# Optimization experiments

Hardware: AMD Instinct MI355X
Metric: run time of the kernel (lower is better)

## Reference

```python
import jax, jax.numpy as jnp
import numpy as np

B = 16            # batch of graphs
N = 512           # n_node
D = 32            # embedding_dim
MAXN = 16         # max_neighbors
E = MAXN * (N - 1)   # 8176 edges per graph
SLEFT = N * D
FSS = 601         # full_support_size
NA = N - 1        # num_actions (so one-hot rows == B*n_node)
IN0 = D + 1       # sa feature dim
NTOT = B * N


def _gat(x, snd, rcv, W, a_src, a_dst, b):
    # single-head GATConv, add_self_loops=False
    h = x @ W                                            # [BN, C]
    e = (h * a_src).sum(-1)[snd] + (h * a_dst).sum(-1)[rcv]
    e = jnp.where(e > 0, e, 0.2 * e)                     # LeakyReLU(0.2)
    m = jax.ops.segment_max(e, rcv, num_segments=NTOT)   # segment softmax
    m = jnp.where(jnp.isfinite(m), m, 0.0)
    ee = jnp.exp(e - m[rcv])
    den = jax.ops.segment_sum(ee, rcv, num_segments=NTOT)
    alpha = ee / (den[rcv] + 1e-16)
    return jax.ops.segment_sum(alpha[:, None] * h[snd], rcv, num_segments=NTOT) + b


def _ln(x, s, o):
    # hk.LayerNorm(axis=-2): normalize over node axis, scale/offset over features
    x3 = x.reshape(B, N, -1)
    mu = x3.mean(axis=1, keepdims=True)
    var = ((x3 - mu) ** 2).mean(axis=1, keepdims=True)
    return ((x3 - mu) * jax.lax.rsqrt(var + 1e-5) * s + o).reshape(B * N, -1)


def _gat_params(key, din, dout):
    k1, k2, k3 = jax.random.split(key, 3)
    sc = 1.0 / np.sqrt(din)
    return (jax.random.normal(k1, (din, dout), jnp.float32) * sc,
            jax.random.normal(k2, (dout,), jnp.float32) * sc,
            jax.random.normal(k3, (dout,), jnp.float32) * sc,
            jnp.zeros((dout,), jnp.float32))


def setup_inputs():
    key = jax.random.key(0)
    ks = jax.random.split(key, 4)
    nodes = jax.random.normal(ks[0], (B, SLEFT), jnp.float32)
    snd = jax.random.randint(ks[1], (B, E), 0, N).astype(jnp.float32)
    rcv = jax.random.randint(ks[2], (B, E), 0, N).astype(jnp.float32)
    ns = jnp.concatenate([nodes, snd, rcv], axis=1)      # [B, SLEFT + 2E]
    a = jax.random.randint(ks[3], (B,), 0, NA + 1)
    inp = {"ns": ns, "a": a}
    dims = [(IN0, 4 * D), (4 * D, 2 * D), (2 * D, 2 * D), (2 * D, D)]
    rdims = [(IN0, FSS), (FSS, FSS), (FSS, FSS), (FSS, FSS)]
    for i, (di, do) in enumerate(dims, 1):
        W, asrc, adst, b = _gat_params(jax.random.fold_in(key, 100 + i), di, do)
        inp.update({f"W{i}": W, f"a{i}s": asrc, f"a{i}d": adst, f"b{i}": b})
        if i < 4:
            inp.update({f"s{i}": jnp.ones((do,), jnp.float32), f"o{i}": jnp.zeros((do,), jnp.float32)})
    for i, (di, do) in enumerate(rdims, 1):
        W, asrc, adst, b = _gat_params(jax.random.fold_in(key, 200 + i), di, do)
        inp.update({f"rW{i}": W, f"ra{i}s": asrc, f"ra{i}d": adst, f"rb{i}": b})
        if i < 4:
            inp.update({f"rs{i}": jnp.ones((FSS,), jnp.float32), f"ro{i}": jnp.zeros((FSS,), jnp.float32)})
    return inp


def reference(ns, a,
              W1, a1s, a1d, b1, s1, o1,
              W2, a2s, a2d, b2, s2, o2,
              W3, a3s, a3d, b3, s3, o3,
              W4, a4s, a4d, b4,
              rW1, ra1s, ra1d, rb1, rs1, ro1,
              rW2, ra2s, ra2d, rb2, rs2, ro2,
              rW3, ra3s, ra3d, rb3, rs3, ro3,
              rW4, ra4s, ra4d, rb4):
    # gbatch: offset per-graph indices into one big graph
    off = (jnp.arange(B, dtype=jnp.int32) * N)[:, None]
    snd = (ns[:, SLEFT:SLEFT + E].astype(jnp.int32) + off).reshape(-1)
    rcv = (ns[:, SLEFT + E:SLEFT + 2 * E].astype(jnp.int32) + off).reshape(-1)
    nodes = ns[:, :SLEFT].reshape(B * N, D)
    sa = jnp.concatenate([nodes, jax.nn.one_hot(a, NA + 1).reshape(-1, 1)], axis=1)
    # reward head
    r = jax.nn.relu(_ln(_gat(sa, snd, rcv, rW1, ra1s, ra1d, rb1), rs1, ro1))
    r = jax.nn.relu(_ln(_gat(r, snd, rcv, rW2, ra2s, ra2d, rb2), rs2, ro2))
    r = jax.nn.relu(_ln(_gat(r, snd, rcv, rW3, ra3s, ra3d, rb3), rs3, ro3))
    r = _gat(r, snd, rcv, rW4, ra4s, ra4d, rb4).reshape(B, N, FSS).sum(axis=1)
    # next-state head
    f = jax.nn.relu(_ln(_gat(sa, snd, rcv, W1, a1s, a1d, b1), s1, o1))
    f = jax.nn.relu(_ln(_gat(f, snd, rcv, W2, a2s, a2d, b2), s2, o2))
    f = jax.nn.relu(_ln(_gat(f, snd, rcv, W3, a3s, a3d, b3), s3, o3))
    f = _gat(f, snd, rcv, W4, a4s, a4d, b4).reshape(B, N * D)
    ns_new = jnp.concatenate([f, ns[:, SLEFT:]], axis=1)
    return (r, ns_new)
```

## Files before the change

kernel.cpp:

```cpp
#include <hip/hip_runtime.h>
#include <math.h>

#define B_ 16
#define N_ 512
#define D_ 32
#define E_ 8176
#define SLEFT_ 16384
#define FSS_ 601
#define BN_ (B_*N_)
#define BE_ (B_*E_)
#define NSROW_ (SLEFT_ + 2*E_)
#define OUT_R_ (B_*FSS_)
#define HLD_ 768
#define CAP_ 128
#define KXB_ 736

typedef __attribute__((ext_vector_type(8))) short short8;
typedef __attribute__((ext_vector_type(4))) float f32x4;

typedef __attribute__((address_space(3))) uint lds_uint;
typedef __attribute__((address_space(1))) const uint g_uint;

__device__ __forceinline__ void gl_lds16(const ushort* gp, ushort* lp) {
  __builtin_amdgcn_global_load_lds((g_uint*)gp, (lds_uint*)lp, 16, 0, 0);
}

__device__ __forceinline__ ushort f2b(float f) {
  uint u = __builtin_bit_cast(uint, f);
  u += 0x7FFFu + ((u >> 16) & 1u);
  return (ushort)(u >> 16);
}
__device__ __forceinline__ float b2f(ushort h) {
  return __builtin_bit_cast(float, ((uint)h) << 16);
}


struct SetupP {
  const float* ns; const int* a;
  int* cnt; int* bins; ushort* sa;
  const float* Wr[4]; const float* Wn[4]; ushort* T[4];
};

__global__ __launch_bounds__(256) void k_setup(SetupP p) {
  __shared__ float tile[32][33];
  int blk = blockIdx.x;
  if (blk < 511) {
    int idx = blk*256 + threadIdx.x;
    if (idx >= BE_) return;
    int b = idx / E_;
    int j = idx - b*E_;
    const float* row = p.ns + (size_t)b*NSROW_;
    int s = (int)row[SLEFT_ + j];
    int r = (int)row[SLEFT_ + E_ + j];
    int dst = b*N_ + r;
    int pos = atomicAdd(&p.cnt[dst], 1);
    if (pos < CAP_) p.bins[(size_t)dst*CAP_ + pos] = b*N_ + s;
    return;
  }
  if (blk < 2559) {
    int idx = (blk-511)*256 + threadIdx.x;
    int v = idx >> 6, c = idx & 63;
    int b = v >> 9, n = v & 511;
    float val = 0.f;
    if (c < 32)       val = p.ns[(size_t)b*NSROW_ + n*32 + c];
    else if (c == 32) val = (p.a[b]==n) ? 1.f : 0.f;
    p.sa[idx] = f2b(val);
    return;
  }
  int t = blk - 2559;
  int s, base, KP, DINR, DINN, DOUTN, KOFF;
  if (t < 48)        { s=0; base=0;    KP=64;  DINR=33;  DINN=33;  DOUTN=128; KOFF=0;   }
  else if (t < 600)  { s=1; base=48;   KP=736; DINR=601; DINN=128; DOUTN=64;  KOFF=608; }
  else if (t < 1104) { s=2; base=600;  KP=672; DINR=601; DINN=64;  DOUTN=64;  KOFF=608; }
  else               { s=3; base=1104; KP=672; DINR=601; DINN=64;  DOUTN=32;  KOFF=608; }
  int ti = t - base;
  int kt = ti / 24, nt = ti - kt*24;
  int k0 = kt*32, n0 = nt*32;
  int tid = threadIdx.x;
  int cc = tid & 31, rr = tid >> 5;
  #pragma unroll
  for (int it=0; it<4; it++) {
    int k = k0 + it*8 + rr;
    int n = n0 + cc;
    float v = 0.f;
    if (n < 640) { if (n < 601 && k < DINR) v = p.Wr[s][(size_t)k*601 + n]; }
    else { int nn = n-640, kk = k-KOFF;
           if (nn < DOUTN && kk >= 0 && kk < DINN) v = p.Wn[s][(size_t)kk*DOUTN + nn]; }
    tile[it*8+rr][cc] = v;
  }
  __syncthreads();
  #pragma unroll
  for (int it=0; it<4; it++) {
    int n = n0 + it*8 + rr;
    int k = k0 + cc;
    p.T[s][(size_t)n*KP + k] = f2b(tile[cc][it*8+rr]);
  }
}


__global__ __launch_bounds__(256) void k_gemm(const ushort* __restrict__ A,
                                              const ushort* __restrict__ Bt,
                                              ushort* __restrict__ C,
                                              float* __restrict__ esed,
                                              const float* __restrict__ asr,
                                              const float* __restrict__ adr,
                                              const float* __restrict__ asn,
                                              const float* __restrict__ adn,
                                              const float* __restrict__ mulb,
                                              const float* __restrict__ addb,
                                              int Kpad, int dn,
                                              int kRewEnd, int kNextBeg, int useLN) {
  __shared__ ushort Asm[2][64*32];
  __shared__ ushort Bsm[2][128*32];
  __shared__ float Lm[KXB_], La[KXB_];
  int tid = threadIdx.x;
  int rowBase = blockIdx.y * 64;
  int colBase = blockIdx.x * 128;
  int kBeg = (blockIdx.x == 5) ? kNextBeg : 0;
  int kEnd = (blockIdx.x == 5) ? Kpad : kRewEnd;
  int wave = tid >> 6, lane = tid & 63;
  int wr = (wave >> 1) * 32, wc = (wave & 1) * 64;
  int lm = lane & 15, lk = (lane >> 4) * 8;

  f32x4 acc[2][4];
  #pragma unroll
  for (int i=0;i<2;i++)
    #pragma unroll
    for (int j=0;j<4;j++) acc[i][j] = (f32x4){0.f,0.f,0.f,0.f};

  int t0 = tid, t1 = tid + 256;
  int ar = t0 >> 2, ac8 = (t0 & 3) * 8;
  const ushort* Bg0 = Bt + (size_t)(colBase + (t0>>2))*Kpad + (t0&3)*8;
  const ushort* Bg1 = Bt + (size_t)(colBase + (t1>>2))*Kpad + (t1&3)*8;
  ushort* Bl0 = &Bsm[0][t0*8];
  ushort* Bl1 = &Bsm[0][t1*8];
  ushort* Al0 = &Asm[0][t0*8];
  const int BSTEP = 128*32, ASTEP = 64*32;

  const ushort* Ag_lds = A + (size_t)(rowBase + ar)*Kpad + ac8;
  int koff = (blockIdx.x == 5) ? 32 : 0;
  const ushort* Ag_vg  = A + (size_t)(rowBase + ar)*HLD_ + koff;

  if (useLN) {
    int b = rowBase >> 9;
    for (int i = tid; i < KXB_; i += 256) {
      Lm[i] = mulb[(size_t)b*KXB_ + i];
      La[i] = addb[(size_t)b*KXB_ + i];
    }
    __syncthreads();
  }

  gl_lds16(Bg0 + kBeg, Bl0);
  gl_lds16(Bg1 + kBeg, Bl1);
  if (useLN) {
    short8 av = *(const short8*)&Ag_vg[kBeg + ac8];
    short8 ov;
    #pragma unroll
    for (int q=0;q<8;q++) {
      float x = b2f((ushort)av[q]);
      int kk = kBeg + ac8 + q;
      float y = x * Lm[kk] + La[kk];
      y = y > 0.f ? y : 0.f;
      ov[q] = (short)f2b(y);
    }
    *(short8*)Al0 = ov;
  } else {
    gl_lds16(Ag_lds + kBeg, Al0);
  }
  __syncthreads();

  int cur = 0;
  for (int k0 = kBeg; k0 < kEnd; k0 += 32) {
    int nxt = cur ^ 1;
    bool more = (k0 + 32) < kEnd;
    short8 avn = short8{};
    if (more) {
      gl_lds16(Bg0 + k0 + 32, Bl0 + nxt*BSTEP);
      gl_lds16(Bg1 + k0 + 32, Bl1 + nxt*BSTEP);
      if (useLN) avn = *(const short8*)&Ag_vg[k0 + 32 + ac8];
      else       gl_lds16(Ag_lds + k0 + 32, Al0 + nxt*ASTEP);
    }
    const ushort* As = &Asm[cur][0];
    const ushort* Bs = &Bsm[cur][0];
    short8 af[2], bfr[4];
    #pragma unroll
    for (int i=0;i<2;i++) af[i]  = *(const short8*)&As[(wr + i*16 + lm)*32 + lk];
    #pragma unroll
    for (int j=0;j<4;j++) bfr[j] = *(const short8*)&Bs[(wc + j*16 + lm)*32 + lk];
    #pragma unroll
    for (int i=0;i<2;i++)
      #pragma unroll
      for (int j=0;j<4;j++)
        acc[i][j] = __builtin_amdgcn_mfma_f32_16x16x32_bf16(af[i], bfr[j], acc[i][j], 0,0,0);
    if (more && useLN) {
      short8 ov;
      #pragma unroll
      for (int q=0;q<8;q++) {
        float x = b2f((ushort)avn[q]);
        int kk = k0 + 32 + ac8 + q;
        float y = x * Lm[kk] + La[kk];
        y = y > 0.f ? y : 0.f;
        ov[q] = (short)f2b(y);
      }
      *(short8*)(Al0 + nxt*ASTEP) = ov;
    }
    __syncthreads();
    cur = nxt;
  }

  float asv[4], adv[4];
  #pragma unroll
  for (int j=0;j<4;j++) {
    int col = colBase + wc + j*16 + lm;
    float s = 0.f, d = 0.f;
    if (col < 601)      { s = asr[col];     d = adr[col]; }
    else if (col >= 640 && col - 640 < dn) { s = asn[col-640]; d = adn[col-640]; }
    asv[j] = s; adv[j] = d;
  }
  int cr = lane >> 4;
  int ct2 = blockIdx.x*2 + (wc >> 6);
  float* esp = (ct2 < 10) ? esed : esed + 2*BN_;
  #pragma unroll
  for (int i=0;i<2;i++) {
    #pragma unroll
    for (int j=0;j<4;j++) {
      int col = colBase + wc + j*16 + lm;
      #pragma unroll
      for (int g=0; g<4; g++) {
        int row = rowBase + wr + i*16 + cr*4 + g;
        C[(size_t)row*HLD_ + col] = f2b(acc[i][j][g]);
      }
    }
    #pragma unroll
    for (int g=0; g<4; g++) {
      float se = 0.f, sd = 0.f;
      #pragma unroll
      for (int j=0;j<4;j++) { se += acc[i][j][g]*asv[j]; sd += acc[i][j][g]*adv[j]; }
      #pragma unroll
      for (int o=1;o<16;o<<=1) { se += __shfl_xor(se,o,64); sd += __shfl_xor(sd,o,64); }
      if (lm == 0) {
        int row = rowBase + wr + i*16 + cr*4 + g;
        atomicAdd(&esp[row], se);
        atomicAdd(&esp[BN_ + row], sd);
      }
    }
  }
}


__global__ __launch_bounds__(256) void k_agg(const ushort* __restrict__ h,
                                             const float* __restrict__ esed,
                                             const int* __restrict__ cnt,
                                             const int* __restrict__ bins,
                                             const float* __restrict__ bias_r,
                                             const float* __restrict__ bias_n,
                                             ushort* __restrict__ g,
                                             int dn) {
  const float* es_r = esed;
  const float* ed_r = esed + BN_;
  const float* es_n = esed + 2*BN_;
  const float* ed_n = esed + 3*BN_;
  int wid = threadIdx.x>>6, lane = threadIdx.x&63;
  int bid = blockIdx.x;
  int xcd = bid & 7, slot = bid >> 3;
  int graph = xcd + ((slot >> 7) << 3);
  int v = graph*512 + (slot & 127)*4 + wid;
  int s0 = v * CAP_;
  int deg = cnt[v]; if (deg > CAP_) deg = CAP_;
  float edr = ed_r[v], edn = ed_n[v];

  int nch = (640 + dn + 7) >> 3;
  int ch0 = lane, ch1 = lane + 64;
  bool a1 = ch1 < nch;
  bool c1r = ch1 < 80;
  float acc0[8], acc1[8];
  #pragma unroll
  for (int q=0;q<8;q++){ acc0[q]=0.f; acc1[q]=0.f; }

  if (deg <= 64) {
    bool has = lane < deg;
    int u = 0; float er = -__builtin_inff(), en = -__builtin_inff();
    if (has) {
      u = bins[s0 + lane];
      er = es_r[u] + edr; er = er > 0.f ? er : 0.2f*er;
      en = es_n[u] + edn; en = en > 0.f ? en : 0.2f*en;
    }
    float mr = er, mn = en;
    #pragma unroll
    for (int o=32;o;o>>=1) { mr = fmaxf(mr, __shfl_xor(mr,o,64)); mn = fmaxf(mn, __shfl_xor(mn,o,64)); }
    float pr = has ? __expf(er - mr) : 0.f;
    float pn = has ? __expf(en - mn) : 0.f;
    float dr = pr, dnm = pn;
    #pragma unroll
    for (int o=32;o;o>>=1) { dr += __shfl_xor(dr,o,64); dnm += __shfl_xor(dnm,o,64); }
    pr *= 1.f/(dr + 1e-16f);
    pn *= 1.f/(dnm + 1e-16f);

    for (int t0 = 0; t0 < deg; t0 += 4) {
      int nt = deg - t0; if (nt > 4) nt = 4;
      short8 va[4], vb[4];
      float w0[4], w1[4];
      #pragma unroll
      for (int q=0;q<4;q++) {
        if (q < nt) {
          int uu = __shfl(u, t0+q, 64);
          w0[q] = __shfl(pr, t0+q, 64);
          w1[q] = __shfl(pn, t0+q, 64);
          const ushort* hp = h + (size_t)uu*HLD_;
          va[q] = *(const short8*)&hp[ch0*8];
          vb[q] = a1 ? *(const short8*)&hp[ch1*8] : short8{};
        } else {
          w0[q] = 0.f; w1[q] = 0.f; va[q] = short8{}; vb[q] = short8{};
        }
      }
      #pragma unroll
      for (int q=0;q<4;q++) {
        #pragma unroll
        for (int r=0;r<8;r++) acc0[r] += w0[q] * b2f((ushort)va[q][r]);
        if (a1) {
          float wv = c1r ? w0[q] : w1[q];
          #pragma unroll
          for (int r=0;r<8;r++) acc1[r] += wv * b2f((ushort)vb[q][r]);
        }
      }
    }
  } else {
    int e0 = s0 + deg;
    float mr = -__builtin_inff(), mn = -__builtin_inff();
    for (int j = s0 + lane; j < e0; j += 64) {
      int u = bins[j];
      float er = es_r[u] + edr; er = er>0.f?er:0.2f*er;
      float en = es_n[u] + edn; en = en>0.f?en:0.2f*en;
      mr = fmaxf(mr, er); mn = fmaxf(mn, en);
    }
    #pragma unroll
    for (int o=32;o;o>>=1) { mr=fmaxf(mr,__shfl_xor(mr,o,64)); mn=fmaxf(mn,__shfl_xor(mn,o,64)); }
    float dr=0.f, dnm=0.f;
    for (int j = s0 + lane; j < e0; j += 64) {
      int u = bins[j];
      float er = es_r[u] + edr; er = er>0.f?er:0.2f*er;
      float en = es_n[u] + edn; en = en>0.f?en:0.2f*en;
      dr += __expf(er-mr); dnm += __expf(en-mn);
    }
    #pragma unroll
    for (int o=32;o;o>>=1) { dr+=__shfl_xor(dr,o,64); dnm+=__shfl_xor(dnm,o,64); }
    float ir = 1.f/(dr+1e-16f), in_ = 1.f/(dnm+1e-16f);
    for (int j = s0; j < e0; ++j) {
      int uu = bins[j];
      float er = es_r[uu] + edr; er = er>0.f?er:0.2f*er;
      float en = es_n[uu] + edn; en = en>0.f?en:0.2f*en;
      float wr2 = __expf(er-mr)*ir, wn2 = __expf(en-mn)*in_;
      const ushort* hp = h + (size_t)uu*HLD_;
      short8 hv = *(const short8*)&hp[ch0*8];
      #pragma unroll
      for (int q=0;q<8;q++) acc0[q] += wr2 * b2f((ushort)hv[q]);
      if (a1) {
        short8 hv2 = *(const short8*)&hp[ch1*8];
        float wv = c1r ? wr2 : wn2;
        #pragma unroll
        for (int q=0;q<8;q++) acc1[q] += wv * b2f((ushort)hv2[q]);
      }
    }
  }

  ushort* gv = g + (size_t)v*HLD_;
  {
    int cb = ch0*8;
    short8 ov;
    #pragma unroll
    for (int q=0;q<8;q++) ov[q] = (short)f2b(acc0[q] + bias_r[cb+q]);
    *(short8*)&gv[cb] = ov;
  }
  if (a1) {
    int cb = ch1*8;
    short8 ov;
    #pragma unroll
    for (int q=0;q<8;q++) {
      int c = cb+q;
      float val;
      if (c < 601)                         val = acc1[q] + bias_r[c];
      else if (c >= 640 && (c-640) < dn)   val = acc1[q] + bias_n[c-640];
      else                                 val = 0.f;
      ov[q] = (short)f2b(val);
    }
    *(short8*)&gv[cb] = ov;
  }
}


__global__ __launch_bounds__(256) void k_lnfin(const ushort* __restrict__ g,
                                               const float* __restrict__ scr,
                                               const float* __restrict__ ofr,
                                               const float* __restrict__ scn,
                                               const float* __restrict__ ofn,
                                               float* __restrict__ mulb,
                                               float* __restrict__ addb,
                                               int dn) {
  int b = blockIdx.y;
  int lc = threadIdx.x & 63, r0 = threadIdx.x >> 6;
  int xb = blockIdx.x*64 + lc;
  bool inrange = xb < KXB_;
  int gcol = (xb < 608) ? xb : xb + 32;
  float s = 0.f, q = 0.f;
  if (inrange) {
    const ushort* gp = g + (size_t)(b*N_)*HLD_ + gcol;
    #pragma unroll 4
    for (int i = 0; i < 128; ++i) {
      int n = r0*128 + i;
      float x = b2f(gp[(size_t)n*HLD_]);
      s += x; q += x*x;
    }
  }
  __shared__ float S[4][64], Q[4][64];
  S[r0][lc]=s; Q[r0][lc]=q; __syncthreads();
  if (r0 == 0 && inrange) {
    float ts = S[0][lc]+S[1][lc]+S[2][lc]+S[3][lc];
    float tq = Q[0][lc]+Q[1][lc]+Q[2][lc]+Q[3][lc];
    bool valid; float scale, offs;
    if (xb < 608) { valid = xb < 601;
                    scale = valid ? scr[xb] : 0.f; offs = valid ? ofr[xb] : 0.f; }
    else { int cn = xb - 608; valid = cn < dn;
           scale = valid ? scn[cn] : 0.f; offs = valid ? ofn[cn] : 0.f; }
    float mul = 0.f, add = 0.f;
    if (valid) {
      float mu = ts*(1.f/N_);
      float var = tq*(1.f/N_) - mu*mu;
      float rs = rsqrtf(var+1e-5f);
      mul = rs*scale;
      add = offs - mu*rs*scale;
    }
    mulb[(size_t)b*KXB_ + xb] = mul;
    addb[(size_t)b*KXB_ + xb] = add;
  }
}


__global__ __launch_bounds__(256) void k_rsum(const ushort* __restrict__ g,
                                              float* __restrict__ rsp) {
  int b = blockIdx.y, z = blockIdx.z; int n0 = z*64;
  int lc = threadIdx.x & 63, r0 = threadIdx.x>>6;
  int c = blockIdx.x*64 + lc;
  float s = 0.f;
  if (c < FSS_) {
    #pragma unroll 4
    for (int i=0;i<16;i++) {
      int n = n0 + r0*16 + i;
      s += b2f(g[(size_t)(b*N_+n)*HLD_ + c]);
    }
  }
  __shared__ float S[4][64];
  S[r0][lc]=s; __syncthreads();
  if (r0==0 && c<FSS_)
    rsp[((size_t)z*B_ + b)*FSS_ + c] = S[0][lc]+S[1][lc]+S[2][lc]+S[3][lc];
}


__global__ __launch_bounds__(256) void k_final(const float* __restrict__ rsp,
                                               const ushort* __restrict__ g,
                                               const float* __restrict__ ns,
                                               float* __restrict__ out) {
  int idx = blockIdx.x*256+threadIdx.x;
  if (idx < OUT_R_) {
    int b = idx / FSS_, c = idx - b*FSS_;
    float s = 0.f;
    #pragma unroll
    for (int z=0;z<8;z++) s += rsp[((size_t)z*B_ + b)*FSS_ + c];
    out[idx] = s;
  } else {
    int j2 = idx - OUT_R_;
    if (j2 >= B_*NSROW_) return;
    int b = j2 / NSROW_; int j = j2 - b*NSROW_;
    float v;
    if (j < SLEFT_) {
      int n = j >> 5, c = j & 31;
      v = b2f(g[(size_t)(b*N_+n)*HLD_ + 640 + c]);
    } else {
      v = ns[(size_t)b*NSROW_ + j];
    }
    out[idx] = v;
  }
}


extern "C" void kernel_launch(void* const* d_in, const int* in_sizes, int n_in,
                              void* d_out, int out_size, void* d_ws, size_t ws_size,
                              hipStream_t stream) {
  const float* ns = (const float*)d_in[0];
  const int*   a  = (const int*)d_in[1];

  const float *W[4], *As[4], *Ad[4], *Bb[4], *Sc[3], *Of[3];
  const float *rW[4], *rAs[4], *rAd[4], *rBb[4], *rSc[3], *rOf[3];
  int p = 2;
  for (int i=0;i<4;i++){
    W[i]=(const float*)d_in[p++]; As[i]=(const float*)d_in[p++];
    Ad[i]=(const float*)d_in[p++]; Bb[i]=(const float*)d_in[p++];
    if (i<3){ Sc[i]=(const float*)d_in[p++]; Of[i]=(const float*)d_in[p++]; }
  }
  for (int i=0;i<4;i++){
    rW[i]=(const float*)d_in[p++]; rAs[i]=(const float*)d_in[p++];
    rAd[i]=(const float*)d_in[p++]; rBb[i]=(const float*)d_in[p++];
    if (i<3){ rSc[i]=(const float*)d_in[p++]; rOf[i]=(const float*)d_in[p++]; }
  }

  char* w = (char*)d_ws;
  auto carve = [&](size_t bytes)->void* {
    void* r = (void*)w;
    w += (bytes + 255) & ~(size_t)255;
    return r;
  };
  ushort* hbuf = (ushort*)carve((size_t)BN_*HLD_*2);
  ushort* gbuf = (ushort*)carve((size_t)BN_*HLD_*2);
  ushort* sabf = (ushort*)carve((size_t)BN_*64*2);
  int* cnt     = (int*)carve((size_t)(BN_ + 4*4*BN_)*4);
  float* esedL = (float*)(cnt + BN_);
  int* bins    = (int*)carve((size_t)BN_*CAP_*4);
  float* mulb  = (float*)carve((size_t)B_*KXB_*4);
  float* addb  = (float*)carve((size_t)B_*KXB_*4);
  float* rsp   = (float*)carve((size_t)8*B_*FSS_*4);
  ushort* Wt[4];
  Wt[0] = (ushort*)carve((size_t)768*64*2);
  Wt[1] = (ushort*)carve((size_t)768*736*2);
  Wt[2] = (ushort*)carve((size_t)768*672*2);
  Wt[3] = (ushort*)carve((size_t)768*672*2);

  float* out = (float*)d_out;

  hipMemsetAsync(cnt, 0, (size_t)(BN_ + 16*BN_)*4, stream);

  SetupP sp;
  sp.ns = ns; sp.a = a; sp.cnt = cnt; sp.bins = bins; sp.sa = sabf;
  for (int i=0;i<4;i++){ sp.Wr[i]=rW[i]; sp.Wn[i]=W[i]; sp.T[i]=Wt[i]; }
  k_setup<<<4167, 256, 0, stream>>>(sp);

  dim3 ggrid(6, BN_/64);

  int Kp[4]   = { 64, 736, 672, 672 };
  int dns[4]  = { 128, 64, 64, 32 };
  int kRe[4]  = { 64, 608, 608, 608 };
  int kNb[4]  = { 0, 608, 608, 608 };

  for (int L=0; L<4; ++L) {
    float* esed = esedL + (size_t)L*4*BN_;
    const ushort* Ain = (L==0) ? sabf : gbuf;
    k_gemm<<<ggrid, 256, 0, stream>>>(Ain, Wt[L], hbuf, esed,
                                      rAs[L], rAd[L], As[L], Ad[L],
                                      mulb, addb, Kp[L], dns[L],
                                      kRe[L], kNb[L], (L==0)?0:1);
    k_agg<<<BN_/4, 256, 0, stream>>>(hbuf, esed, cnt, bins,
                                     rBb[L], Bb[L], gbuf, dns[L]);
    if (L < 3) {
      k_lnfin<<<dim3(12, B_), 256, 0, stream>>>(gbuf, rSc[L], rOf[L], Sc[L], Of[L],
                                                mulb, addb, dns[L]);
    }
  }

  k_rsum<<<dim3(10, B_, 8), 256, 0, stream>>>(gbuf, rsp);
  k_final<<<(OUT_R_ + B_*NSROW_ + 255)/256, 256, 0, stream>>>(rsp, gbuf, ns, out);
}
```

Measured before the change: 376.9 us.

## Remap GEMM grid to XCD-aware 1D order and drop LDS double buffering

The GEMM launch becomes a 1D grid of 768 blocks. Each block id is remapped so that groups of row tiles sharing a column tile are likely placed on the same XCD (bid&7), which is meant to improve L2 reuse of the weight and activation tiles. The double-buffered LDS prefetch pipeline is also replaced with a single-buffer load-sync-compute-sync loop. That halves LDS use, which may raise occupancy, but global loads no longer overlap with the MFMA work.

```diff
diff --git a/kernel.cpp b/kernel.cpp
--- a/kernel.cpp
+++ b/kernel.cpp
@@ -110,14 +110,18 @@
                                               const float* __restrict__ addb,
                                               int Kpad, int dn,
                                               int kRewEnd, int kNextBeg, int useLN) {
-  __shared__ ushort Asm[2][64*32];
-  __shared__ ushort Bsm[2][128*32];
+  __shared__ ushort Asm[64*32];
+  __shared__ ushort Bsm[128*32];
   __shared__ float Lm[KXB_], La[KXB_];
   int tid = threadIdx.x;
-  int rowBase = blockIdx.y * 64;
-  int colBase = blockIdx.x * 128;
-  int kBeg = (blockIdx.x == 5) ? kNextBeg : 0;
-  int kEnd = (blockIdx.x == 5) ? Kpad : kRewEnd;
+  int bid = blockIdx.x;
+  int x = bid & 7, q = bid >> 3;
+  int rbl = q & 15, cb = q >> 4;
+  int grp = x + ((rbl >> 3) << 3);
+  int rowBase = (grp*8 + (rbl & 7)) * 64;
+  int colBase = cb * 128;
+  int kBeg = (cb == 5) ? kNextBeg : 0;
+  int kEnd = (cb == 5) ? Kpad : kRewEnd;
   int wave = tid >> 6, lane = tid & 63;
   int wr = (wave >> 1) * 32, wc = (wave & 1) * 64;
   int lm = lane & 15, lk = (lane >> 4) * 8;
@@ -132,13 +136,12 @@
   int ar = t0 >> 2, ac8 = (t0 & 3) * 8;
   const ushort* Bg0 = Bt + (size_t)(colBase + (t0>>2))*Kpad + (t0&3)*8;
   const ushort* Bg1 = Bt + (size_t)(colBase + (t1>>2))*Kpad + (t1&3)*8;
-  ushort* Bl0 = &Bsm[0][t0*8];
-  ushort* Bl1 = &Bsm[0][t1*8];
-  ushort* Al0 = &Asm[0][t0*8];
-  const int BSTEP = 128*32, ASTEP = 64*32;
+  ushort* Bl0 = &Bsm[t0*8];
+  ushort* Bl1 = &Bsm[t1*8];
+  ushort* Al0 = &Asm[t0*8];
 
   const ushort* Ag_lds = A + (size_t)(rowBase + ar)*Kpad + ac8;
-  int koff = (blockIdx.x == 5) ? 32 : 0;
+  int koff = (cb == 5) ? 32 : 0;
   const ushort* Ag_vg  = A + (size_t)(rowBase + ar)*HLD_ + koff;
 
   if (useLN) {
@@ -150,62 +153,35 @@
     __syncthreads();
   }
 
-  gl_lds16(Bg0 + kBeg, Bl0);
-  gl_lds16(Bg1 + kBeg, Bl1);
-  if (useLN) {
-    short8 av = *(const short8*)&Ag_vg[kBeg + ac8];
-    short8 ov;
-    #pragma unroll
-    for (int q=0;q<8;q++) {
-      float x = b2f((ushort)av[q]);
-      int kk = kBeg + ac8 + q;
-      float y = x * Lm[kk] + La[kk];
-      y = y > 0.f ? y : 0.f;
-      ov[q] = (short)f2b(y);
-    }
-    *(short8*)Al0 = ov;
-  } else {
-    gl_lds16(Ag_lds + kBeg, Al0);
-  }
-  __syncthreads();
-
-  int cur = 0;
   for (int k0 = kBeg; k0 < kEnd; k0 += 32) {
-    int nxt = cur ^ 1;
-    bool more = (k0 + 32) < kEnd;
-    short8 avn = short8{};
-    if (more) {
-      gl_lds16(Bg0 + k0 + 32, Bl0 + nxt*BSTEP);
-      gl_lds16(Bg1 + k0 + 32, Bl1 + nxt*BSTEP);
-      if (useLN) avn = *(const short8*)&Ag_vg[k0 + 32 + ac8];
-      else       gl_lds16(Ag_lds + k0 + 32, Al0 + nxt*ASTEP);
-    }
-    const ushort* As = &Asm[cur][0];
-    const ushort* Bs = &Bsm[cur][0];
+    gl_lds16(Bg0 + k0, Bl0);
+    gl_lds16(Bg1 + k0, Bl1);
+    if (useLN) {
+      short8 av = *(const short8*)&Ag_vg[k0 + ac8];
+      short8 ov;
+      #pragma unroll
+      for (int q2=0;q2<8;q2++) {
+        float xv = b2f((ushort)av[q2]);
+        float y = xv * Lm[k0 + ac8 + q2] + La[k0 + ac8 + q2];
+        y = y > 0.f ? y : 0.f;
+        ov[q2] = (short)f2b(y);
+      }
+      *(short8*)Al0 = ov;
+    } else {
+      gl_lds16(Ag_lds + k0, Al0);
+    }
+    __syncthreads();
     short8 af[2], bfr[4];
     #pragma unroll
-    for (int i=0;i<2;i++) af[i]  = *(const short8*)&As[(wr + i*16 + lm)*32 + lk];
-    #pragma unroll
-    for (int j=0;j<4;j++) bfr[j] = *(const short8*)&Bs[(wc + j*16 + lm)*32 + lk];
+    for (int i=0;i<2;i++) af[i]  = *(short8*)&Asm[(wr + i*16 + lm)*32 + lk];
+    #pragma unroll
+    for (int j=0;j<4;j++) bfr[j] = *(short8*)&Bsm[(wc + j*16 + lm)*32 + lk];
     #pragma unroll
     for (int i=0;i<2;i++)
       #pragma unroll
       for (int j=0;j<4;j++)
         acc[i][j] = __builtin_amdgcn_mfma_f32_16x16x32_bf16(af[i], bfr[j], acc[i][j], 0,0,0);
-    if (more && useLN) {
-      short8 ov;
-      #pragma unroll
-      for (int q=0;q<8;q++) {
-        float x = b2f((ushort)avn[q]);
-        int kk = k0 + 32 + ac8 + q;
-        float y = x * Lm[kk] + La[kk];
-        y = y > 0.f ? y : 0.f;
-        ov[q] = (short)f2b(y);
-      }
-      *(short8*)(Al0 + nxt*ASTEP) = ov;
-    }
     __syncthreads();
-    cur = nxt;
   }
 
   float asv[4], adv[4];
@@ -218,7 +194,7 @@
     asv[j] = s; adv[j] = d;
   }
   int cr = lane >> 4;
-  int ct2 = blockIdx.x*2 + (wc >> 6);
+  int ct2 = cb*2 + (wc >> 6);
   float* esp = (ct2 < 10) ? esed : esed + 2*BN_;
   #pragma unroll
   for (int i=0;i<2;i++) {
@@ -532,8 +508,6 @@
   for (int i=0;i<4;i++){ sp.Wr[i]=rW[i]; sp.Wn[i]=W[i]; sp.T[i]=Wt[i]; }
   k_setup<<<4167, 256, 0, stream>>>(sp);
 
-  dim3 ggrid(6, BN_/64);
-
   int Kp[4]   = { 64, 736, 672, 672 };
   int dns[4]  = { 128, 64, 64, 32 };
   int kRe[4]  = { 64, 608, 608, 608 };
@@ -542,10 +516,10 @@
   for (int L=0; L<4; ++L) {
     float* esed = esedL + (size_t)L*4*BN_;
     const ushort* Ain = (L==0) ? sabf : gbuf;
-    k_gemm<<<ggrid, 256, 0, stream>>>(Ain, Wt[L], hbuf, esed,
-                                      rAs[L], rAd[L], As[L], Ad[L],
-                                      mulb, addb, Kp[L], dns[L],
-                                      kRe[L], kNb[L], (L==0)?0:1);
+    k_gemm<<<768, 256, 0, stream>>>(Ain, Wt[L], hbuf, esed,
+                                    rAs[L], rAd[L], As[L], Ad[L],
+                                    mulb, addb, Kp[L], dns[L],
+                                    kRe[L], kNb[L], (L==0)?0:1);
     k_agg<<<BN_/4, 256, 0, stream>>>(hbuf, esed, cnt, bins,
                                      rBb[L], Bb[L], gbuf, dns[L]);
     if (L < 3) {
```

Result: faster. 363.5 us (-3.6%).
